# Performance work log

Hardware: AMD Instinct MI355X
Metric: run time of the kernel (lower is better)

The kernel has to match this reference:

```python
import jax, jax.numpy as jnp
import numpy as np

B_GRAPHS = 16      # number of graphs in batch
NPG = 8192         # nodes per graph
N = B_GRAPHS * NPG # 131072 total nodes
F_DIM = 64         # node feature dim
K_CLUST = 16       # n_clusters
DEG = 32           # avg degree
E = N * DEG        # 4,194,304 edges


def setup_inputs() -> dict:
    key = jax.random.key(0)
    k1, k2, k3, k4, k5 = jax.random.split(key, 5)
    x = jax.random.normal(k1, (N, F_DIM), jnp.float32)
    W = jax.random.normal(k2, (F_DIM, K_CLUST), jnp.float32) / np.sqrt(F_DIM)
    b = jnp.zeros((K_CLUST,), jnp.float32)
    # edges constrained within each graph -> block-diagonal adjacency (PyG batching)
    g = jnp.repeat(jnp.arange(B_GRAPHS, dtype=jnp.int32), E // B_GRAPHS)
    edge_row = g * NPG + jax.random.randint(k3, (E,), 0, NPG, jnp.int32)
    edge_col = g * NPG + jax.random.randint(k4, (E,), 0, NPG, jnp.int32)
    edge_weight = jax.random.uniform(k5, (E,), jnp.float32)
    return {"x": x, "W": W, "b": b, "edge_weight": edge_weight,
            "edge_row": edge_row, "edge_col": edge_col, "num_graphs": B_GRAPHS}


def _forward(x, W, b, edge_weight, edge_row, edge_col, num_graphs):
    Ntot, Fd = x.shape
    K = W.shape[1]
    Bn = num_graphs
    n = Ntot // Bn  # equal-size graphs (ptr = n * arange(B+1))

    s = x @ W + b                                   # [N,K] cluster logits
    xb = x.reshape(Bn, n, Fd)
    sb = s.reshape(Bn, n, K)
    # out_x = selu(s^T @ x_bd), block b = s_b^T x_b, then hsplit_and_vstack -> [B*K, F]
    out_x = jax.nn.selu(jnp.einsum('bnk,bnf->bkf', sb, xb)).reshape(Bn * K, Fd)

    ss = jax.nn.softmax(s, axis=-1)                 # softmaxed assignments
    ssb = ss.reshape(Bn, n, K)

    # degree d = adj.sum(axis=0)  (column sums over COO edges)
    d = jax.ops.segment_sum(edge_weight, edge_col, num_segments=Ntot)   # [N]
    m2 = d.reshape(Bn, n).sum(1)                    # total degree per graph [B]

    # A @ C via edge scatter: (A C)[row] += w * C[col]
    AC = jax.ops.segment_sum(edge_weight[:, None] * ss[edge_col], edge_row,
                             num_segments=Ntot)     # [N,K]
    # out_adj blocks: C_b^T A_b C_b  -> [B,K,K]
    out_adj = jnp.einsum('bnk,bnl->bkl', ssb, AC.reshape(Bn, n, K))

    # dS_b = C_b^T d_b  (Ca/Cb blocks); normalizer gets m_inv twice in torch code
    dS = jnp.einsum('bn,bnk->bk', d.reshape(Bn, n), ssb)                # [B,K]
    spectral_loss = -jnp.mean(jnp.einsum('bkk->b', out_adj) / m2
                              - (dS ** 2).sum(1) / (m2 ** 2))

    sqrt_K = jnp.sqrt(jnp.float32(K))
    cluster_size = ssb.sum(1)                        # [B,K]
    cluster_loss = jnp.mean(jnp.sqrt((cluster_size ** 2).sum(1)) / n * sqrt_K - 1.0)

    # CC blocks: C_b^T C_b; ortho = mean_b || CC_b/||CC_b||_F - I/sqrt(K) ||_F
    CC = jnp.einsum('bnk,bnl->bkl', ssb, ssb)        # [B,K,K]
    CC_norm = jnp.sqrt((CC ** 2).sum((1, 2)))        # Frobenius norm per block
    eye_div_k = jnp.eye(K, dtype=x.dtype) / sqrt_K
    ortho_loss = jnp.mean(jnp.sqrt(
        ((CC / CC_norm[:, None, None] - eye_div_k) ** 2).sum((1, 2))))

    # mask diagonal and degree-normalize pooled adjacency
    oa = out_adj * (1.0 - jnp.eye(K, dtype=x.dtype))
    dd = jnp.sqrt(oa.sum(2)) + 1e-12                 # row sums per block [B,K]
    out_adj_norm = oa / (dd[:, :, None] * dd[:, None, :])

    return out_x, out_adj_norm, spectral_loss, cluster_loss, ortho_loss


def reference(x, W, b, edge_weight, edge_row, edge_col, num_graphs):
    return _forward(x, W, b, edge_weight, edge_row, edge_col, num_graphs)
```

## Files before the change

kernel.cpp:

```cpp
#include <hip/hip_runtime.h>
#include <math.h>
#include <stdint.h>

#define F_DIM 64
#define K_CL 16
#define B_GR 16
#define SR32 68

typedef _Float16 h16;
using f16x8 = __attribute__((ext_vector_type(8))) _Float16;
using f16x2 = __attribute__((ext_vector_type(2))) _Float16;
using f32x4 = __attribute__((ext_vector_type(4))) float;

union HU { h16 f; unsigned short u; };
union PU { uint32_t u; f16x2 v; };
union H8 { f16x8 v; uint32_t u[4]; };

__global__ __launch_bounds__(256) void k_fused(
    const float* __restrict__ x, const float* __restrict__ W, const float* __restrict__ bvec,
    uint32_t* __restrict__ ssq, float* __restrict__ outx, float* __restrict__ CCb)
{
    __shared__ float Wl[F_DIM * K_CL];
    __shared__ float bl[K_CL];
    __shared__ __align__(16) float Ss[256 * 20];
    __shared__ __align__(16) float Cs[256 * 20];
    __shared__ float CCl[256];

    int t = threadIdx.x;
    for (int idx = t; idx < F_DIM * K_CL; idx += 256) Wl[idx] = W[idx];
    if (t < K_CL) bl[t] = bvec[t];
    CCl[t] = 0.f;
    __syncthreads();

    int wid = t >> 6, lane = t & 63;
    int bid = blockIdx.x;

    {
        size_t i = (size_t)bid * 256 + t;
        float s[16];
#pragma unroll
        for (int k = 0; k < 16; ++k) s[k] = bl[k];

        const float4* xp = reinterpret_cast<const float4*>(x + i * F_DIM);
#pragma unroll
        for (int j = 0; j < 16; ++j) {
            float4 q = xp[j];
            float xf[4] = {q.x, q.y, q.z, q.w};
#pragma unroll
            for (int ff = 0; ff < 4; ++ff) {
                int f = j * 4 + ff;
                float xv = xf[ff];
                const float4* wr = reinterpret_cast<const float4*>(&Wl[f * K_CL]);
                float4 w0 = wr[0], w1 = wr[1], w2 = wr[2], w3 = wr[3];
                s[0]  += xv * w0.x; s[1]  += xv * w0.y; s[2]  += xv * w0.z; s[3]  += xv * w0.w;
                s[4]  += xv * w1.x; s[5]  += xv * w1.y; s[6]  += xv * w1.z; s[7]  += xv * w1.w;
                s[8]  += xv * w2.x; s[9]  += xv * w2.y; s[10] += xv * w2.z; s[11] += xv * w2.w;
                s[12] += xv * w3.x; s[13] += xv * w3.y; s[14] += xv * w3.z; s[15] += xv * w3.w;
            }
        }

        float4* sp = reinterpret_cast<float4*>(&Ss[t * 20]);
        sp[0] = make_float4(s[0], s[1], s[2], s[3]);
        sp[1] = make_float4(s[4], s[5], s[6], s[7]);
        sp[2] = make_float4(s[8], s[9], s[10], s[11]);
        sp[3] = make_float4(s[12], s[13], s[14], s[15]);

        float m = s[0];
#pragma unroll
        for (int k = 1; k < 16; ++k) m = fmaxf(m, s[k]);
        float sum = 0.f;
#pragma unroll
        for (int k = 0; k < 16; ++k) { s[k] = __expf(s[k] - m); sum += s[k]; }
        float inv = 1.0f / sum;
#pragma unroll
        for (int k = 0; k < 16; ++k) s[k] *= inv;

        float4* cp = reinterpret_cast<float4*>(&Cs[t * 20]);
        cp[0] = make_float4(s[0], s[1], s[2], s[3]);
        cp[1] = make_float4(s[4], s[5], s[6], s[7]);
        cp[2] = make_float4(s[8], s[9], s[10], s[11]);
        cp[3] = make_float4(s[12], s[13], s[14], s[15]);

        uint32_t g[4];
#pragma unroll
        for (int i4 = 0; i4 < 4; ++i4) {
            uint32_t acc = 0;
#pragma unroll
            for (int j4 = 0; j4 < 4; ++j4) {
                HU h; h.f = (h16)s[i4 * 4 + j4];
                uint32_t u = h.u;
                uint32_t b = (u + 0x7Fu + ((u >> 7) & 1u)) >> 8;
                acc |= (b & 0xFFu) << (8 * j4);
            }
            g[i4] = acc;
        }
        *reinterpret_cast<uint4*>(ssq + i * 4) = make_uint4(g[0], g[1], g[2], g[3]);
    }

    float accx[16];
#pragma unroll
    for (int k = 0; k < 16; ++k) accx[k] = 0.f;
    float accc[4] = {0.f, 0.f, 0.f, 0.f};
    int g4 = lane >> 4, l = lane & 15;
    size_t xbase = ((size_t)bid * 256 + wid * 64) * F_DIM;

    for (int j = 0; j < 64; ++j) {
        int node = wid * 64 + j;
        float xv = x[xbase + (size_t)j * F_DIM + lane];
        const float4* sp = reinterpret_cast<const float4*>(&Ss[node * 20]);
        float4 s0 = sp[0], s1 = sp[1], s2 = sp[2], s3 = sp[3];
        accx[0]  += s0.x * xv; accx[1]  += s0.y * xv; accx[2]  += s0.z * xv; accx[3]  += s0.w * xv;
        accx[4]  += s1.x * xv; accx[5]  += s1.y * xv; accx[6]  += s1.z * xv; accx[7]  += s1.w * xv;
        accx[8]  += s2.x * xv; accx[9]  += s2.y * xv; accx[10] += s2.z * xv; accx[11] += s2.w * xv;
        accx[12] += s3.x * xv; accx[13] += s3.y * xv; accx[14] += s3.z * xv; accx[15] += s3.w * xv;

        float ssl = Cs[node * 20 + l];
        float4 sq = *reinterpret_cast<const float4*>(&Cs[node * 20 + g4 * 4]);
        accc[0] += sq.x * ssl;
        accc[1] += sq.y * ssl;
        accc[2] += sq.z * ssl;
        accc[3] += sq.w * ssl;
    }

#pragma unroll
    for (int j4 = 0; j4 < 4; ++j4)
        atomicAdd(&CCl[(g4 * 4 + j4) * 16 + l], accc[j4]);
    __syncthreads();

    float* redx = Ss;
#pragma unroll
    for (int k = 0; k < 16; ++k) redx[wid * 1024 + k * 64 + lane] = accx[k];
    __syncthreads();

    int g = bid >> 5;
    float* dst = outx + g * (K_CL * F_DIM);
#pragma unroll
    for (int it = 0; it < 4; ++it) {
        int idx = t + it * 256;
        float v = redx[idx] + redx[1024 + idx] + redx[2048 + idx] + redx[3072 + idx];
        atomicAdd(dst + idx, v);
    }
    atomicAdd(&CCb[g * 256 + t], CCl[t]);
}

__global__ __launch_bounds__(256) void k_edge(
    const int* __restrict__ erow, const int* __restrict__ ecol, const float* __restrict__ ew,
    const uint32_t* __restrict__ ssq, float* __restrict__ oadj,
    int edges_per_block, int edges_per_graph, int nmask)
{
    __shared__ float CCl[256];
    __shared__ __align__(16) uint32_t AB[4][16 * SR32];
    int t = threadIdx.x;
    CCl[t] = 0.f;
    __syncthreads();

    int bid = blockIdx.x;
    int xcd = bid & 7;
    int slot = bid >> 3;
    int graph = xcd + 8 * (slot & 1);
    int chunk = slot >> 1;

    int wid = t >> 6, lane = t & 63;
    int q4 = lane >> 4, mm = lane & 15;
    uint32_t* ABw = AB[wid];

    int epw = edges_per_block >> 2;
    size_t base = (size_t)graph * edges_per_graph
                + (size_t)chunk * edges_per_block
                + (size_t)wid * epw;

    f32x4 acc = {0.f, 0.f, 0.f, 0.f};

    for (int e0 = 0; e0 < epw; e0 += 64) {
        size_t eb = base + e0 + lane;
        int   r = erow[eb] & nmask;
        int   c = ecol[eb] & nmask;
        float w = ew[eb];

        uint4 ga = *reinterpret_cast<const uint4*>(ssq + (size_t)r * 4);
        uint4 gb = *reinterpret_cast<const uint4*>(ssq + (size_t)c * 4);

        uint32_t pa[8], pb[8];
        uint32_t gaw[4] = {ga.x, ga.y, ga.z, ga.w};
        uint32_t gbw[4] = {gb.x, gb.y, gb.z, gb.w};
#pragma unroll
        for (int i4 = 0; i4 < 4; ++i4) {
            pa[2 * i4]     = (gaw[i4] << 8) & 0xFF00FF00u;
            pa[2 * i4 + 1] =  gaw[i4]       & 0xFF00FF00u;
            pb[2 * i4]     = (gbw[i4] << 8) & 0xFF00FF00u;
            pb[2 * i4 + 1] =  gbw[i4]       & 0xFF00FF00u;
        }

        HU wh; wh.f = (h16)w;
        PU wp; wp.u = (uint32_t)wh.u | ((uint32_t)wh.u << 16);
#pragma unroll
        for (int i8 = 0; i8 < 8; ++i8) {
            PU a; a.u = pa[i8];
            a.v = a.v * wp.v;
            pa[i8] = a.u;
        }

#pragma unroll
        for (int i4 = 0; i4 < 4; ++i4) {
            uint32_t alo = pa[2 * i4], ahi = pa[2 * i4 + 1];
            uint32_t blo = pb[2 * i4], bhi = pb[2 * i4 + 1];
            ABw[(4 * i4 + 0) * SR32 + lane] = (alo & 0xFFFFu) | (blo << 16);
            ABw[(4 * i4 + 1) * SR32 + lane] = (ahi & 0xFFFFu) | (bhi << 16);
            ABw[(4 * i4 + 2) * SR32 + lane] = (alo >> 16) | (bhi & 0u) | (blo & 0xFFFF0000u);
            ABw[(4 * i4 + 3) * SR32 + lane] = (ahi >> 16) | (bhi & 0xFFFF0000u);
        }

#pragma unroll
        for (int h = 0; h < 2; ++h) {
            const uint32_t* rowp = &ABw[mm * SR32 + h * 32 + q4 * 8];
            uint4 p0 = *reinterpret_cast<const uint4*>(rowp);
            uint4 p1 = *reinterpret_cast<const uint4*>(rowp + 4);
            H8 Af, Bf;
            Af.u[0] = (p0.x & 0xFFFFu) | (p0.y << 16);
            Bf.u[0] = (p0.x >> 16)     | (p0.y & 0xFFFF0000u);
            Af.u[1] = (p0.z & 0xFFFFu) | (p0.w << 16);
            Bf.u[1] = (p0.z >> 16)     | (p0.w & 0xFFFF0000u);
            Af.u[2] = (p1.x & 0xFFFFu) | (p1.y << 16);
            Bf.u[2] = (p1.x >> 16)     | (p1.y & 0xFFFF0000u);
            Af.u[3] = (p1.z & 0xFFFFu) | (p1.w << 16);
            Bf.u[3] = (p1.z >> 16)     | (p1.w & 0xFFFF0000u);
            acc = __builtin_amdgcn_mfma_f32_16x16x32_f16(Af.v, Bf.v, acc, 0, 0, 0);
        }
    }

#pragma unroll
    for (int rg = 0; rg < 4; ++rg)
        atomicAdd(&CCl[(q4 * 4 + rg) * 16 + mm], acc[rg]);
    __syncthreads();
    atomicAdd(oadj + graph * 256 + t, CCl[t]);
}

__global__ __launch_bounds__(256) void k_final(
    const float* __restrict__ outx, const float* __restrict__ oadj,
    const float* __restrict__ CCb, float* __restrict__ out, int npg)
{
    int t = threadIdx.x;
    int gid = blockIdx.x * 256 + t;
    {
        float v = outx[gid];
        float r = (v > 0.f) ? (1.0507009873554805f * v)
                            : (1.0507009873554805f * 1.6732632423543772f * (__expf(v) - 1.0f));
        out[gid] = r;
    }

    if (blockIdx.x != 0) return;

    int b = t >> 4, k = t & 15;
    const float* oar = oadj + b * 256 + k * 16;
    const float* ccr = CCb + b * 256 + k * 16;

    float rowsum_off = 0.f, trace_c = 0.f, rowsum_all = 0.f, fro2 = 0.f, colsum = 0.f;
    float csv = 0.f;
#pragma unroll
    for (int l = 0; l < 16; ++l) {
        float v = oar[l];
        rowsum_all += v;
        if (l == k) trace_c = v; else rowsum_off += v;
        float c = ccr[l];
        fro2 += c * c;
        csv += c;
        colsum += oadj[b * 256 + l * 16 + k];
    }
    float dd = sqrtf(rowsum_off) + 1e-12f;
    __shared__ float ddl[B_GR * K_CL];
    ddl[t] = dd;

    float ds2 = colsum * colsum, cs2 = csv * csv;
    float tr = trace_c, m2 = rowsum_all;
#pragma unroll
    for (int msk = 8; msk >= 1; msk >>= 1) {
        tr   += __shfl_xor(tr,   msk, 16);
        ds2  += __shfl_xor(ds2,  msk, 16);
        cs2  += __shfl_xor(cs2,  msk, 16);
        fro2 += __shfl_xor(fro2, msk, 16);
        m2   += __shfl_xor(m2,   msk, 16);
    }
    float invfro = 1.0f / sqrtf(fro2);
    float osum = 0.f;
#pragma unroll
    for (int l = 0; l < 16; ++l) {
        float v = ccr[l] * invfro - ((l == k) ? 0.25f : 0.f);
        osum += v * v;
    }
#pragma unroll
    for (int msk = 8; msk >= 1; msk >>= 1) osum += __shfl_xor(osum, msk, 16);

    __shared__ float sp_s[B_GR], cl_s[B_GR], or_s[B_GR];
    if (k == 0) {
        sp_s[b] = tr / m2 - ds2 / (m2 * m2);
        cl_s[b] = sqrtf(cs2) / (float)npg * 4.0f - 1.0f;
        or_s[b] = sqrtf(osum);
    }
    __syncthreads();
    if (t == 0) {
        float a = 0.f, c = 0.f, o = 0.f;
        for (int i = 0; i < B_GR; ++i) { a += sp_s[i]; c += cl_s[i]; o += or_s[i]; }
        out[20480] = -a / 16.f;
        out[20481] = c / 16.f;
        out[20482] = o / 16.f;
    }

#pragma unroll
    for (int l = 0; l < 16; ++l) {
        float v = (l == k) ? 0.f : oar[l] / (dd * ddl[b * 16 + l]);
        out[16384 + b * 256 + k * 16 + l] = v;
    }
}

extern "C" void kernel_launch(void* const* d_in, const int* in_sizes, int n_in,
                              void* d_out, int out_size, void* d_ws, size_t ws_size,
                              hipStream_t stream)
{
    const float* x    = (const float*)d_in[0];
    const float* W    = (const float*)d_in[1];
    const float* bvec = (const float*)d_in[2];
    const float* ew   = (const float*)d_in[3];
    const int* erow   = (const int*)d_in[4];
    const int* ecol   = (const int*)d_in[5];

    int Ntot = in_sizes[0] / F_DIM;
    size_t E = (size_t)in_sizes[3];
    int npg  = Ntot / B_GR;
    int edges_per_graph = (int)(E / B_GR);
    int nmask = Ntot - 1;

    const int ADJ_BLOCKS = 2048;
    int edges_per_block = (int)(E / ADJ_BLOCKS);

    char* ws = (char*)d_ws;
    size_t o = 0;
    uint32_t* ssq = (uint32_t*)(ws + o); o += (size_t)Ntot * 16;
    size_t zoff = o;
    float* outx = (float*)(ws + o); o += (size_t)B_GR * 1024 * 4;
    float* oadj = (float*)(ws + o); o += (size_t)B_GR * 256 * 4;
    float* CCb  = (float*)(ws + o); o += (size_t)B_GR * 256 * 4;

    hipMemsetAsync(ws + zoff, 0, o - zoff, stream);

    k_fused<<<Ntot / 256, 256, 0, stream>>>(x, W, bvec, ssq, outx, CCb);
    k_edge<<<ADJ_BLOCKS, 256, 0, stream>>>(erow, ecol, ew, ssq, oadj,
                                           edges_per_block, edges_per_graph, nmask);
    k_final<<<64, 256, 0, stream>>>(outx, oadj, CCb, (float*)d_out, npg);
}
```

Baseline: 176.4 us.

## Software-pipeline edge index and gather loads; store softmax tile as packed fp16

The edge kernel now prefetches edge indices two iterations ahead and the gathered quantized assignment rows one iteration ahead. This hides the dependent global-load latency of the index-then-gather chain behind the MFMA work. Separately, the fused kernel stores the softmax tile in shared memory as packed fp16 pairs instead of padded fp32. That shrinks LDS use, which may help occupancy, and adds a barrier before the reduction loop. The costs are more registers for the in-flight prefetches and some precision loss in the CC accumulation.

```diff
diff --git a/kernel.cpp b/kernel.cpp
--- a/kernel.cpp
+++ b/kernel.cpp
@@ -23,7 +23,7 @@
     __shared__ float Wl[F_DIM * K_CL];
     __shared__ float bl[K_CL];
     __shared__ __align__(16) float Ss[256 * 20];
-    __shared__ __align__(16) float Cs[256 * 20];
+    __shared__ uint32_t Csu[256 * 9];
     __shared__ float CCl[256];
 
     int t = threadIdx.x;
@@ -75,11 +75,13 @@
 #pragma unroll
         for (int k = 0; k < 16; ++k) s[k] *= inv;
 
-        float4* cp = reinterpret_cast<float4*>(&Cs[t * 20]);
-        cp[0] = make_float4(s[0], s[1], s[2], s[3]);
-        cp[1] = make_float4(s[4], s[5], s[6], s[7]);
-        cp[2] = make_float4(s[8], s[9], s[10], s[11]);
-        cp[3] = make_float4(s[12], s[13], s[14], s[15]);
+#pragma unroll
+        for (int p = 0; p < 8; ++p) {
+            PU u;
+            u.v[0] = (h16)s[2 * p];
+            u.v[1] = (h16)s[2 * p + 1];
+            Csu[t * 9 + p] = u.u;
+        }
 
         uint32_t g[4];
 #pragma unroll
@@ -96,6 +98,7 @@
         }
         *reinterpret_cast<uint4*>(ssq + i * 4) = make_uint4(g[0], g[1], g[2], g[3]);
     }
+    __syncthreads();
 
     float accx[16];
 #pragma unroll
@@ -114,12 +117,15 @@
         accx[8]  += s2.x * xv; accx[9]  += s2.y * xv; accx[10] += s2.z * xv; accx[11] += s2.w * xv;
         accx[12] += s3.x * xv; accx[13] += s3.y * xv; accx[14] += s3.z * xv; accx[15] += s3.w * xv;
 
-        float ssl = Cs[node * 20 + l];
-        float4 sq = *reinterpret_cast<const float4*>(&Cs[node * 20 + g4 * 4]);
-        accc[0] += sq.x * ssl;
-        accc[1] += sq.y * ssl;
-        accc[2] += sq.z * ssl;
-        accc[3] += sq.w * ssl;
+        const uint32_t* cp = &Csu[node * 9];
+        PU pl; pl.u = cp[l >> 1];
+        float ssl = (float)pl.v[l & 1];
+        PU q0; q0.u = cp[g4 * 2];
+        PU q1; q1.u = cp[g4 * 2 + 1];
+        accc[0] += (float)q0.v[0] * ssl;
+        accc[1] += (float)q0.v[1] * ssl;
+        accc[2] += (float)q1.v[0] * ssl;
+        accc[3] += (float)q1.v[1] * ssl;
     }
 
 #pragma unroll
@@ -165,24 +171,41 @@
     uint32_t* ABw = AB[wid];
 
     int epw = edges_per_block >> 2;
+    int iters = epw >> 6;
     size_t base = (size_t)graph * edges_per_graph
                 + (size_t)chunk * edges_per_block
                 + (size_t)wid * epw;
 
+    const uint4* ssqv = reinterpret_cast<const uint4*>(ssq);
     f32x4 acc = {0.f, 0.f, 0.f, 0.f};
 
-    for (int e0 = 0; e0 < epw; e0 += 64) {
-        size_t eb = base + e0 + lane;
-        int   r = erow[eb] & nmask;
-        int   c = ecol[eb] & nmask;
-        float w = ew[eb];
-
-        uint4 ga = *reinterpret_cast<const uint4*>(ssq + (size_t)r * 4);
-        uint4 gb = *reinterpret_cast<const uint4*>(ssq + (size_t)c * 4);
+    int r_c, c_c, r_n = 0, c_n = 0;
+    float w_c, w_n = 0.f;
+    uint4 ga_c, gb_c;
+
+    {
+        size_t e0 = base + lane;
+        r_c = erow[e0] & nmask; c_c = ecol[e0] & nmask; w_c = ew[e0];
+        ga_c = ssqv[r_c]; gb_c = ssqv[c_c];
+        if (iters > 1) {
+            size_t e1 = e0 + 64;
+            r_n = erow[e1] & nmask; c_n = ecol[e1] & nmask; w_n = ew[e1];
+        }
+    }
+
+    for (int i = 0; i < iters; ++i) {
+        uint4 ga_n, gb_n;
+        if (i + 1 < iters) { ga_n = ssqv[r_n]; gb_n = ssqv[c_n]; }
+        int r_nn = 0, c_nn = 0;
+        float w_nn = 0.f;
+        if (i + 2 < iters) {
+            size_t e2 = base + (size_t)(i + 2) * 64 + lane;
+            r_nn = erow[e2] & nmask; c_nn = ecol[e2] & nmask; w_nn = ew[e2];
+        }
 
         uint32_t pa[8], pb[8];
-        uint32_t gaw[4] = {ga.x, ga.y, ga.z, ga.w};
-        uint32_t gbw[4] = {gb.x, gb.y, gb.z, gb.w};
+        uint32_t gaw[4] = {ga_c.x, ga_c.y, ga_c.z, ga_c.w};
+        uint32_t gbw[4] = {gb_c.x, gb_c.y, gb_c.z, gb_c.w};
 #pragma unroll
         for (int i4 = 0; i4 < 4; ++i4) {
             pa[2 * i4]     = (gaw[i4] << 8) & 0xFF00FF00u;
@@ -191,7 +214,7 @@
             pb[2 * i4 + 1] =  gbw[i4]       & 0xFF00FF00u;
         }
 
-        HU wh; wh.f = (h16)w;
+        HU wh; wh.f = (h16)w_c;
         PU wp; wp.u = (uint32_t)wh.u | ((uint32_t)wh.u << 16);
 #pragma unroll
         for (int i8 = 0; i8 < 8; ++i8) {
@@ -206,7 +229,7 @@
             uint32_t blo = pb[2 * i4], bhi = pb[2 * i4 + 1];
             ABw[(4 * i4 + 0) * SR32 + lane] = (alo & 0xFFFFu) | (blo << 16);
             ABw[(4 * i4 + 1) * SR32 + lane] = (ahi & 0xFFFFu) | (bhi << 16);
-            ABw[(4 * i4 + 2) * SR32 + lane] = (alo >> 16) | (bhi & 0u) | (blo & 0xFFFF0000u);
+            ABw[(4 * i4 + 2) * SR32 + lane] = (alo >> 16) | (blo & 0xFFFF0000u);
             ABw[(4 * i4 + 3) * SR32 + lane] = (ahi >> 16) | (bhi & 0xFFFF0000u);
         }
 
@@ -226,6 +249,10 @@
             Bf.u[3] = (p1.z >> 16)     | (p1.w & 0xFFFF0000u);
             acc = __builtin_amdgcn_mfma_f32_16x16x32_f16(Af.v, Bf.v, acc, 0, 0, 0);
         }
+
+        r_c = r_n; c_c = c_n; w_c = w_n;
+        ga_c = ga_n; gb_c = gb_n;
+        r_n = r_nn; c_n = c_nn; w_n = w_nn;
     }
 
 #pragma unroll
```

Measured after the change: 172.2 us. -2.4%, faster.
